# Optimization experiments

Measured on AMD Instinct MI355X. Metric: run time of the kernel, lower is better.

## Reference

```python
import math
import jax, jax.numpy as jnp
import numpy as np

B, L, D_MODEL = 2, 2048, 1024
N_HEAD, HEAD_DIM = 16, 64
ATT_SCALE = 1.0  # divisor is sqrt(head_dim ** attention_scale)


def setup_inputs() -> dict:
    key = jax.random.key(0)
    ks = jax.random.split(key, 6)
    HD = N_HEAD * HEAD_DIM
    # Xavier-uniform style init for projection weights (stored as [in, out])
    def xavier(k, fan_in, fan_out):
        lim = math.sqrt(6.0 / (fan_in + fan_out))
        return jax.random.uniform(k, (fan_in, fan_out), jnp.float32, -lim, lim)
    return {
        "x":  jax.random.normal(ks[0], (B, L, D_MODEL), jnp.float32),
        "Wq": xavier(ks[1], D_MODEL, HD), "bq": jnp.zeros((HD,), jnp.float32),
        "Wk": xavier(ks[2], D_MODEL, HD), "bk": jnp.zeros((HD,), jnp.float32),
        "Wv": xavier(ks[3], D_MODEL, HD), "bv": jnp.zeros((HD,), jnp.float32),
        "Wo": xavier(ks[4], HD, D_MODEL),
        "bo": jax.random.uniform(ks[5], (D_MODEL,), jnp.float32, -1.0 / math.sqrt(HD), 1.0 / math.sqrt(HD)),
    }


def reference(x, Wq, bq, Wk, bk, Wv, bv, Wo, bo):
    b, l, _ = x.shape
    # QKV projections -> [B, L, H, Dh]
    q = (x @ Wq + bq).reshape(b, l, N_HEAD, HEAD_DIM)
    k = (x @ Wk + bk).reshape(b, l, N_HEAD, HEAD_DIM)
    v = (x @ Wv + bv).reshape(b, l, N_HEAD, HEAD_DIM)
    scale = 1.0 / math.sqrt(HEAD_DIM ** ATT_SCALE)
    # Unnormalized (no softmax) attention: (Q K^T / sqrt(Dh)) V
    scores = jnp.einsum("blhd,bmhd->bhlm", q, k) * scale  # [B,H,L,L]
    attn = jnp.einsum("bhlm,bmhd->blhd", scores, v)        # [B,L,H,Dh]
    out = attn.reshape(b, l, N_HEAD * HEAD_DIM) @ Wo + bo  # dispatcher
    return out
```

## Files before the change

kernel.cpp:

```cpp
#include <hip/hip_runtime.h>
#include <stdint.h>

#define B_ 2
#define L_ 2048
#define DM 1024
#define NH 16
#define DH 64
#define M_ (B_*L_)
#define NQKV 3072

typedef short short8 __attribute__((ext_vector_type(8)));
typedef float f32x4 __attribute__((ext_vector_type(4)));

__device__ __forceinline__ unsigned short f2b(float f) {
    union { float f; unsigned int u; } v; v.f = f;
    unsigned int u = v.u;
    return (unsigned short)((u + 0x7fffu + ((u >> 16) & 1u)) >> 16);
}

__device__ __forceinline__ void gld_lds16(const void* g, void* l) {
    __builtin_amdgcn_global_load_lds(
        (const __attribute__((address_space(1))) void*)g,
        (__attribute__((address_space(3))) void*)l, 16, 0, 0);
}

__global__ __launch_bounds__(256)
void setup_kernel(const float* __restrict__ x,
                  const float* __restrict__ Wq, const float* __restrict__ Wk,
                  const float* __restrict__ Wv, const float* __restrict__ Wo,
                  const float* __restrict__ bq, const float* __restrict__ bk,
                  const float* __restrict__ bv,
                  unsigned short* __restrict__ xb, unsigned short* __restrict__ WqkvT,
                  unsigned short* __restrict__ WoT, float* __restrict__ biasq,
                  float* __restrict__ KtV)
{
    __shared__ float tile[32][33];
    const int bid = blockIdx.x;
    const int t = threadIdx.x;

    if (bid < 2048) {
        int i = (bid * 256 + t) * 8;
        float4 a0 = *(const float4*)(x + i);
        float4 a1 = *(const float4*)(x + i + 4);
        uint4 p;
        p.x = (unsigned)f2b(a0.x) | ((unsigned)f2b(a0.y) << 16);
        p.y = (unsigned)f2b(a0.z) | ((unsigned)f2b(a0.w) << 16);
        p.z = (unsigned)f2b(a1.x) | ((unsigned)f2b(a1.y) << 16);
        p.w = (unsigned)f2b(a1.z) | ((unsigned)f2b(a1.w) << 16);
        *(uint4*)(xb + i) = p;
    } else if (bid < 2048 + 4096) {
        int wb = bid - 2048;
        int wi = wb >> 10;
        int tid = wb & 1023;
        const float* W = (wi == 0) ? Wq : (wi == 1) ? Wk : (wi == 2) ? Wv : Wo;
        float s = (wi == 1) ? 0.125f : 1.0f;
        int n0 = (tid & 31) * 32, k0 = (tid >> 5) * 32;
        int r = t >> 3, c4 = (t & 7) << 2;
        float4 v = *(const float4*)(W + (size_t)(k0 + r) * DM + n0 + c4);
        tile[r][c4+0] = v.x; tile[r][c4+1] = v.y; tile[r][c4+2] = v.z; tile[r][c4+3] = v.w;
        __syncthreads();
        uint2 o;
        o.x = (unsigned)f2b(tile[c4+0][r]*s) | ((unsigned)f2b(tile[c4+1][r]*s) << 16);
        o.y = (unsigned)f2b(tile[c4+2][r]*s) | ((unsigned)f2b(tile[c4+3][r]*s) << 16);
        int f = n0 + r;
        size_t drow;
        unsigned short* dst;
        if (wi == 0)      { dst = WqkvT; drow = f; }
        else if (wi == 1) { dst = WqkvT; drow = 1024 + (f >> 6) * 128 + (f & 63); }
        else if (wi == 2) { dst = WqkvT; drow = 1024 + (f >> 6) * 128 + 64 + (f & 63); }
        else              { dst = WoT;   drow = f; }
        *(uint2*)(dst + drow * DM + k0 + c4) = o;
    } else if (bid < 2048 + 4096 + 12) {
        int n = (bid - 6144) * 256 + t;
        float v;
        if (n < 1024) v = bq[n];
        else {
            int kv = (n - 1024) >> 7, r = (n - 1024) & 127;
            v = (r < 64) ? 0.125f * bk[kv * 64 + r] : bv[kv * 64 + (r - 64)];
        }
        biasq[n] = v;
    } else {
        int i = ((bid - 6156) * 256 + t) * 4;
        float4 z; z.x = z.y = z.z = z.w = 0.f;
        *(float4*)(KtV + i) = z;
    }
}

__global__ __launch_bounds__(512, 2)
void qkv_fused_kernel(const unsigned short* __restrict__ A,
                      const unsigned short* __restrict__ Bt,
                      const float* __restrict__ biasq,
                      unsigned short* __restrict__ Qb,
                      float* __restrict__ KtV)
{
    __shared__ __align__(16) char smem[131072];

    const int bid = blockIdx.x;
    const int mt = bid & 15;
    const int nt = bid >> 4;
    const int m0 = mt * 256, n0 = nt * 256;

    const int t = threadIdx.x;
    const int w = t >> 6, lane = t & 63;
    const int quad = lane >> 4, l16 = lane & 15;
    const int wr = w >> 2, wc = w & 3;

    f32x4 acc[8][4];
    #pragma unroll
    for (int i = 0; i < 8; i++)
        #pragma unroll
        for (int j = 0; j < 4; j++)
            #pragma unroll
            for (int r = 0; r < 4; r++) acc[i][j][r] = 0.f;

    auto STAGE = [&](int buf, int kk) {
        #pragma unroll
        for (int p = 0; p < 4; p++) {
            int c = p * 512 + t;
            int row = c >> 3, slot = c & 7;
            int g = slot ^ ((row >> 1) & 7);
            gld_lds16(A + (size_t)(m0 + row) * DM + kk + g * 8,
                      smem + buf * 65536 + p * 8192 + w * 1024);
        }
        #pragma unroll
        for (int p = 0; p < 4; p++) {
            int c = p * 512 + t;
            int row = c >> 3, slot = c & 7;
            int g = slot ^ ((row >> 1) & 7);
            gld_lds16(Bt + (size_t)(n0 + row) * DM + kk + g * 8,
                      smem + buf * 65536 + 32768 + p * 8192 + w * 1024);
        }
    };

    STAGE(0, 0);
    STAGE(1, 64);
    asm volatile("s_waitcnt vmcnt(8)" ::: "memory");
    __builtin_amdgcn_sched_barrier(0);
    __builtin_amdgcn_s_barrier();

    for (int T = 0; T < 16; T++) {
        const char* Ab = smem + (T & 1) * 65536;
        const char* Bb = Ab + 32768;
        #pragma unroll
        for (int kf = 0; kf < 2; kf++) {
            int kc = kf * 4 + quad;
            short8 af[8], bf[4];
            #pragma unroll
            for (int i = 0; i < 8; i++) {
                int am = wr * 128 + i * 16 + l16;
                af[i] = *(const short8*)(Ab + am * 128 + ((kc ^ ((am >> 1) & 7)) << 4));
            }
            #pragma unroll
            for (int j = 0; j < 4; j++) {
                int bn = wc * 64 + j * 16 + l16;
                bf[j] = *(const short8*)(Bb + bn * 128 + ((kc ^ ((bn >> 1) & 7)) << 4));
            }
            #pragma unroll
            for (int i = 0; i < 8; i++)
                #pragma unroll
                for (int j = 0; j < 4; j++)
                    acc[i][j] = __builtin_amdgcn_mfma_f32_16x16x32_bf16(af[i], bf[j], acc[i][j], 0, 0, 0);
        }
        __builtin_amdgcn_sched_barrier(0);
        __builtin_amdgcn_s_barrier();
        if (T < 14) {
            STAGE(T & 1, (T + 2) * 64);
            __builtin_amdgcn_sched_barrier(0);
            asm volatile("s_waitcnt vmcnt(8)" ::: "memory");
        } else {
            asm volatile("s_waitcnt vmcnt(0)" ::: "memory");
        }
        __builtin_amdgcn_sched_barrier(0);
        __builtin_amdgcn_s_barrier();
    }

    #pragma unroll
    for (int j = 0; j < 4; j++) {
        float bv = biasq[n0 + wc * 64 + j * 16 + l16];
        #pragma unroll
        for (int i = 0; i < 8; i++)
            #pragma unroll
            for (int r = 0; r < 4; r++) acc[i][j][r] += bv;
    }

    if (nt < 4) {
        #pragma unroll
        for (int j = 0; j < 4; j++) {
            int col = n0 + wc * 64 + j * 16 + l16;
            #pragma unroll
            for (int i = 0; i < 8; i++) {
                #pragma unroll
                for (int r = 0; r < 4; r++) {
                    int row = m0 + wr * 128 + i * 16 + quad * 4 + r;
                    Qb[(size_t)row * DM + col] = f2b(acc[i][j][r]);
                }
            }
        }
        return;
    }

    #pragma unroll
    for (int j = 0; j < 4; j++) {
        int c = wc * 64 + j * 16 + l16;
        int cs = (c & 7) << 4;
        #pragma unroll
        for (int i = 0; i < 8; i++) {
            int l0 = wr * 128 + i * 16 + quad * 4;
            uint2 o;
            o.x = (unsigned)f2b(acc[i][j][0]) | ((unsigned)f2b(acc[i][j][1]) << 16);
            o.y = (unsigned)f2b(acc[i][j][2]) | ((unsigned)f2b(acc[i][j][3]) << 16);
            *(uint2*)(smem + c * 512 + ((l0 * 2) ^ cs)) = o;
        }
    }
    __builtin_amdgcn_sched_barrier(0);
    __builtin_amdgcn_s_barrier();

    const int hh = w >> 2;
    const int s  = w & 3;
    const int bb = mt >> 3;
    const int h  = (nt - 4) * 2 + hh;

    f32x4 kacc[4];
    #pragma unroll
    for (int j = 0; j < 4; j++)
        #pragma unroll
        for (int r = 0; r < 4; r++) kacc[j][r] = 0.f;

    #pragma unroll
    for (int ks = 0; ks < 8; ks++) {
        int ca = hh * 128 + s * 16 + l16;
        short8 afk = *(const short8*)(smem + ca * 512 + ((ks * 64 + quad * 16) ^ ((ca & 7) << 4)));
        #pragma unroll
        for (int j = 0; j < 4; j++) {
            int cb = hh * 128 + 64 + j * 16 + l16;
            short8 bfk = *(const short8*)(smem + cb * 512 + ((ks * 64 + quad * 16) ^ ((cb & 7) << 4)));
            kacc[j] = __builtin_amdgcn_mfma_f32_16x16x32_bf16(afk, bfk, kacc[j], 0, 0, 0);
        }
    }

    float* dst = KtV + (size_t)(bb * NH + h) * 64 * 64;
    #pragma unroll
    for (int j = 0; j < 4; j++) {
        int col = j * 16 + l16;
        #pragma unroll
        for (int r = 0; r < 4; r++) {
            int row = s * 16 + quad * 4 + r;
            atomicAdd(dst + row * 64 + col, kacc[j][r]);
        }
    }
}

__global__ __launch_bounds__(256)
void zmat_kernel(const unsigned short* __restrict__ WoT, const float* __restrict__ KtV,
                 unsigned short* __restrict__ ZT)
{
    __shared__ __align__(16) unsigned short Asl[64][72];
    __shared__ __align__(16) unsigned short Bsl[64][72];

    const int bh = blockIdx.x, nt0 = blockIdx.y;
    const int b = bh >> 4, h = bh & 15;
    const int t = threadIdx.x;
    const int wave = t >> 6, lane = t & 63;
    const int quad = lane >> 4, l16 = lane & 15;
    const int n0 = nt0 * 64;
    const int row = t >> 2, c0 = (t & 3) << 4;

    const unsigned short* ap = WoT + (size_t)(n0 + row) * DM + h * DH + c0;
    *(uint4*)&Asl[row][c0]     = *(const uint4*)ap;
    *(uint4*)&Asl[row][c0 + 8] = *(const uint4*)(ap + 8);

    const float* kp = KtV + ((size_t)bh * 64 + row) * 64 + c0;
    #pragma unroll
    for (int j = 0; j < 16; j++) Bsl[row][c0 + j] = f2b(kp[j]);
    __syncthreads();

    f32x4 acc[4];
    #pragma unroll
    for (int i = 0; i < 4; i++)
        #pragma unroll
        for (int r = 0; r < 4; r++) acc[i][r] = 0.f;

    #pragma unroll
    for (int ks = 0; ks < 2; ks++) {
        short8 af = *(const short8*)&Asl[wave * 16 + l16][ks * 32 + quad * 8];
        #pragma unroll
        for (int nt = 0; nt < 4; nt++) {
            short8 bfr = *(const short8*)&Bsl[nt * 16 + l16][ks * 32 + quad * 8];
            acc[nt] = __builtin_amdgcn_mfma_f32_16x16x32_bf16(af, bfr, acc[nt], 0, 0, 0);
        }
    }

    unsigned short* zb = ZT + (size_t)b * 1024 * 1024 + (size_t)h * DH;
    #pragma unroll
    for (int nt = 0; nt < 4; nt++) {
        int col = nt * 16 + l16;
        #pragma unroll
        for (int r = 0; r < 4; r++) {
            int zr = n0 + wave * 16 + quad * 4 + r;
            zb[(size_t)zr * 1024 + col] = f2b(acc[nt][r]);
        }
    }
}

__global__ __launch_bounds__(256)
void out_gemm_kernel(const unsigned short* __restrict__ A,
                     const unsigned short* __restrict__ Bt,
                     const float* __restrict__ bias,
                     float* __restrict__ C)
{
    __shared__ __align__(16) unsigned short As[128 * 64];
    __shared__ __align__(16) unsigned short Bs[64 * 64];

    const int bid = blockIdx.x;
    const int xcd = bid & 7, local = bid >> 3;
    const int mt = xcd * 4 + (local & 3);
    const int nt = local >> 2;
    const int m0 = mt * 128, n0 = nt * 64;

    const int t = threadIdx.x;
    const int w = t >> 6, lane = t & 63;
    const int quad = lane >> 4, l16 = lane & 15;

    const unsigned short* Btb = Bt + (size_t)(m0 >> 11) * 1024 * 1024;

    f32x4 acc[2][4];
    #pragma unroll
    for (int i = 0; i < 2; i++)
        #pragma unroll
        for (int j = 0; j < 4; j++)
            #pragma unroll
            for (int r = 0; r < 4; r++) acc[i][j][r] = 0.f;

    for (int kk = 0; kk < DM; kk += 64) {
        #pragma unroll
        for (int p = 0; p < 4; p++) {
            int c = p * 256 + t;
            int row = c >> 3, slot = c & 7;
            int g = slot ^ ((row >> 1) & 7);
            gld_lds16(A + (size_t)(m0 + row) * DM + kk + g * 8,
                      (char*)As + p * 4096 + w * 1024);
        }
        #pragma unroll
        for (int p = 0; p < 2; p++) {
            int c = p * 256 + t;
            int row = c >> 3, slot = c & 7;
            int g = slot ^ ((row >> 1) & 7);
            gld_lds16(Btb + (size_t)(n0 + row) * DM + kk + g * 8,
                      (char*)Bs + p * 4096 + w * 1024);
        }
        __syncthreads();

        #pragma unroll
        for (int ks = 0; ks < 2; ks++) {
            int kc = ks * 4 + quad;
            short8 afr[2], bfr[4];
            #pragma unroll
            for (int i = 0; i < 2; i++) {
                int am = w * 32 + i * 16 + l16;
                afr[i] = *(const short8*)((const char*)As + am * 128 + ((kc ^ ((am >> 1) & 7)) << 4));
            }
            #pragma unroll
            for (int j = 0; j < 4; j++) {
                int bn = j * 16 + l16;
                bfr[j] = *(const short8*)((const char*)Bs + bn * 128 + ((kc ^ ((bn >> 1) & 7)) << 4));
            }
            #pragma unroll
            for (int i = 0; i < 2; i++)
                #pragma unroll
                for (int j = 0; j < 4; j++)
                    acc[i][j] = __builtin_amdgcn_mfma_f32_16x16x32_bf16(afr[i], bfr[j], acc[i][j], 0, 0, 0);
        }
        __syncthreads();
    }

    #pragma unroll
    for (int j = 0; j < 4; j++) {
        int col = n0 + j * 16 + l16;
        float bv = bias[col];
        #pragma unroll
        for (int i = 0; i < 2; i++) {
            #pragma unroll
            for (int r = 0; r < 4; r++) {
                int row = m0 + w * 32 + i * 16 + quad * 4 + r;
                C[(size_t)row * DM + col] = acc[i][j][r] + bv;
            }
        }
    }
}


extern "C" void kernel_launch(void* const* d_in, const int* in_sizes, int n_in,
                              void* d_out, int out_size, void* d_ws, size_t ws_size,
                              hipStream_t stream)
{
    const float* x  = (const float*)d_in[0];
    const float* Wq = (const float*)d_in[1];
    const float* bq = (const float*)d_in[2];
    const float* Wk = (const float*)d_in[3];
    const float* bk = (const float*)d_in[4];
    const float* Wv = (const float*)d_in[5];
    const float* bv = (const float*)d_in[6];
    const float* Wo = (const float*)d_in[7];
    const float* bo = (const float*)d_in[8];

    char* ws = (char*)d_ws;
    unsigned short* xb    = (unsigned short*)(ws);
    unsigned short* WqkvT = (unsigned short*)(ws + (size_t)8  * 1024 * 1024);
    unsigned short* WoT   = (unsigned short*)(ws + (size_t)14 * 1024 * 1024);
    float*          biasq = (float*)         (ws + (size_t)16 * 1024 * 1024);
    unsigned short* Qb    = (unsigned short*)(ws + (size_t)17 * 1024 * 1024);
    unsigned short* ZT    = (unsigned short*)(ws + (size_t)25 * 1024 * 1024);
    float*          KtV   = (float*)         (ws + (size_t)29 * 1024 * 1024);

    setup_kernel<<<6284, 256, 0, stream>>>(x, Wq, Wk, Wv, Wo, bq, bk, bv,
                                           xb, WqkvT, WoT, biasq, KtV);

    qkv_fused_kernel<<<192, 512, 0, stream>>>(xb, WqkvT, biasq, Qb, KtV);

    zmat_kernel<<<dim3(B_ * NH, 16), 256, 0, stream>>>(WoT, KtV, ZT);

    out_gemm_kernel<<<512, 256, 0, stream>>>(Qb, ZT, bo, (float*)d_out);
}
```

Before: 148.1 us.

## Restructure QKV GEMM main loop into triple-buffered K=32 pipeline with interleaved staging

Replaces the double-buffered K=64 main loop of the QKV projection GEMM with a triple-buffered K=32 pipeline that uses one barrier per iteration. Global-to-LDS loads for A and B are split and interleaved between two halves of the MFMA work. s_setprio is raised around the MFMA bursts. The aim is to hide load latency better and to cut barrier count per unit of K. The cost is more iterations, a smaller swizzle width and an extra epilogue barrier before LDS is reused for the transposed K/V write.

Result: faster. 142.2 us (-4.0%).

```diff
diff --git a/kernel.cpp b/kernel.cpp
--- a/kernel.cpp
+++ b/kernel.cpp
@@ -7,7 +7,6 @@
 #define NH 16
 #define DH 64
 #define M_ (B_*L_)
-#define NQKV 3072
 
 typedef short short8 __attribute__((ext_vector_type(8)));
 typedef float f32x4 __attribute__((ext_vector_type(4)));
@@ -113,65 +112,107 @@
             #pragma unroll
             for (int r = 0; r < 4; r++) acc[i][j][r] = 0.f;
 
-    auto STAGE = [&](int buf, int kk) {
-        #pragma unroll
-        for (int p = 0; p < 4; p++) {
-            int c = p * 512 + t;
-            int row = c >> 3, slot = c & 7;
-            int g = slot ^ ((row >> 1) & 7);
-            gld_lds16(A + (size_t)(m0 + row) * DM + kk + g * 8,
-                      smem + buf * 65536 + p * 8192 + w * 1024);
-        }
-        #pragma unroll
-        for (int p = 0; p < 4; p++) {
-            int c = p * 512 + t;
-            int row = c >> 3, slot = c & 7;
-            int g = slot ^ ((row >> 1) & 7);
-            gld_lds16(Bt + (size_t)(n0 + row) * DM + kk + g * 8,
-                      smem + buf * 65536 + 32768 + p * 8192 + w * 1024);
-        }
+    const int c0 = t, c1 = 512 + t;
+    const int row0 = c0 >> 2, g0 = (c0 & 3) ^ ((row0 >> 1) & 3);
+    const int row1 = c1 >> 2, g1 = (c1 & 3) ^ ((row1 >> 1) & 3);
+
+    auto STAGE_A = [&](int buf, int kk) {
+        gld_lds16(A + (size_t)(m0 + row0) * DM + kk + g0 * 8,
+                  smem + buf * 32768 + w * 1024);
+        gld_lds16(A + (size_t)(m0 + row1) * DM + kk + g1 * 8,
+                  smem + buf * 32768 + 8192 + w * 1024);
     };
-
-    STAGE(0, 0);
-    STAGE(1, 64);
-    asm volatile("s_waitcnt vmcnt(8)" ::: "memory");
+    auto STAGE_B = [&](int buf, int kk) {
+        gld_lds16(Bt + (size_t)(n0 + row0) * DM + kk + g0 * 8,
+                  smem + buf * 32768 + 16384 + w * 1024);
+        gld_lds16(Bt + (size_t)(n0 + row1) * DM + kk + g1 * 8,
+                  smem + buf * 32768 + 16384 + 8192 + w * 1024);
+    };
+
+    STAGE_A(0, 0);  STAGE_B(0, 0);
+    STAGE_A(1, 32); STAGE_B(1, 32);
+
+    int cur = 0, st = 2;
+    short8 bf[4], af[4];
+
+    for (int T = 0; T < 31; T++) {
+        asm volatile("s_waitcnt vmcnt(4)" ::: "memory");
+        __builtin_amdgcn_sched_barrier(0);
+        __builtin_amdgcn_s_barrier();
+        __builtin_amdgcn_sched_barrier(0);
+
+        const char* Ab = smem + cur * 32768;
+        const char* Bb = Ab + 16384;
+
+        if (T < 30) STAGE_A(st, (T + 2) * 32);
+        #pragma unroll
+        for (int j = 0; j < 4; j++) {
+            int bn = wc * 64 + j * 16 + l16;
+            bf[j] = *(const short8*)(Bb + bn * 64 + ((quad ^ ((bn >> 1) & 3)) << 4));
+        }
+        #pragma unroll
+        for (int i = 0; i < 4; i++) {
+            int am = wr * 128 + i * 16 + l16;
+            af[i] = *(const short8*)(Ab + am * 64 + ((quad ^ ((am >> 1) & 3)) << 4));
+        }
+        __builtin_amdgcn_s_setprio(1);
+        #pragma unroll
+        for (int i = 0; i < 4; i++)
+            #pragma unroll
+            for (int j = 0; j < 4; j++)
+                acc[i][j] = __builtin_amdgcn_mfma_f32_16x16x32_bf16(af[i], bf[j], acc[i][j], 0, 0, 0);
+        __builtin_amdgcn_s_setprio(0);
+
+        if (T < 30) STAGE_B(st, (T + 2) * 32);
+        #pragma unroll
+        for (int i = 0; i < 4; i++) {
+            int am = wr * 128 + (i + 4) * 16 + l16;
+            af[i] = *(const short8*)(Ab + am * 64 + ((quad ^ ((am >> 1) & 3)) << 4));
+        }
+        __builtin_amdgcn_s_setprio(1);
+        #pragma unroll
+        for (int i = 0; i < 4; i++)
+            #pragma unroll
+            for (int j = 0; j < 4; j++)
+                acc[i + 4][j] = __builtin_amdgcn_mfma_f32_16x16x32_bf16(af[i], bf[j], acc[i + 4][j], 0, 0, 0);
+        __builtin_amdgcn_s_setprio(0);
+
+        cur = (cur == 2) ? 0 : cur + 1;
+        st  = (st  == 2) ? 0 : st  + 1;
+    }
+
+    asm volatile("s_waitcnt vmcnt(0)" ::: "memory");
     __builtin_amdgcn_sched_barrier(0);
     __builtin_amdgcn_s_barrier();
-
-    for (int T = 0; T < 16; T++) {
-        const char* Ab = smem + (T & 1) * 65536;
-        const char* Bb = Ab + 32768;
-        #pragma unroll
-        for (int kf = 0; kf < 2; kf++) {
-            int kc = kf * 4 + quad;
-            short8 af[8], bf[4];
-            #pragma unroll
-            for (int i = 0; i < 8; i++) {
-                int am = wr * 128 + i * 16 + l16;
-                af[i] = *(const short8*)(Ab + am * 128 + ((kc ^ ((am >> 1) & 7)) << 4));
-            }
-            #pragma unroll
-            for (int j = 0; j < 4; j++) {
-                int bn = wc * 64 + j * 16 + l16;
-                bf[j] = *(const short8*)(Bb + bn * 128 + ((kc ^ ((bn >> 1) & 7)) << 4));
-            }
-            #pragma unroll
-            for (int i = 0; i < 8; i++)
-                #pragma unroll
-                for (int j = 0; j < 4; j++)
-                    acc[i][j] = __builtin_amdgcn_mfma_f32_16x16x32_bf16(af[i], bf[j], acc[i][j], 0, 0, 0);
-        }
-        __builtin_amdgcn_sched_barrier(0);
-        __builtin_amdgcn_s_barrier();
-        if (T < 14) {
-            STAGE(T & 1, (T + 2) * 64);
-            __builtin_amdgcn_sched_barrier(0);
-            asm volatile("s_waitcnt vmcnt(8)" ::: "memory");
-        } else {
-            asm volatile("s_waitcnt vmcnt(0)" ::: "memory");
-        }
-        __builtin_amdgcn_sched_barrier(0);
-        __builtin_amdgcn_s_barrier();
+    __builtin_amdgcn_sched_barrier(0);
+    {
+        const char* Ab = smem + cur * 32768;
+        const char* Bb = Ab + 16384;
+        #pragma unroll
+        for (int j = 0; j < 4; j++) {
+            int bn = wc * 64 + j * 16 + l16;
+            bf[j] = *(const short8*)(Bb + bn * 64 + ((quad ^ ((bn >> 1) & 3)) << 4));
+        }
+        #pragma unroll
+        for (int i = 0; i < 4; i++) {
+            int am = wr * 128 + i * 16 + l16;
+            af[i] = *(const short8*)(Ab + am * 64 + ((quad ^ ((am >> 1) & 3)) << 4));
+        }
+        #pragma unroll
+        for (int i = 0; i < 4; i++)
+            #pragma unroll
+            for (int j = 0; j < 4; j++)
+                acc[i][j] = __builtin_amdgcn_mfma_f32_16x16x32_bf16(af[i], bf[j], acc[i][j], 0, 0, 0);
+        #pragma unroll
+        for (int i = 0; i < 4; i++) {
+            int am = wr * 128 + (i + 4) * 16 + l16;
+            af[i] = *(const short8*)(Ab + am * 64 + ((quad ^ ((am >> 1) & 3)) << 4));
+        }
+        #pragma unroll
+        for (int i = 0; i < 4; i++)
+            #pragma unroll
+            for (int j = 0; j < 4; j++)
+                acc[i + 4][j] = __builtin_amdgcn_mfma_f32_16x16x32_bf16(af[i], bf[j], acc[i + 4][j], 0, 0, 0);
     }
 
     #pragma unroll
@@ -198,6 +239,9 @@
         }
         return;
     }
+
+    __builtin_amdgcn_sched_barrier(0);
+    __builtin_amdgcn_s_barrier();
 
     #pragma unroll
     for (int j = 0; j < 4; j++) {
```
